# Performance work log

Hardware: AMD Instinct MI355X
Metric: run time of the kernel (lower is better)

The kernel has to match this reference:

```python
import jax, jax.numpy as jnp
import numpy as np

N, M, D, K = 8192, 16384, 512, 512
RESULT_BLUR = 0.01  # self.result_blur in the original module


def setup_inputs() -> dict:
    key = jax.random.key(0)
    k1, k2, k3, k4 = jax.random.split(key, 4)
    x = jax.random.normal(k1, (N, D), jnp.float32)          # current embeddings (feature_rows)
    cache_emb = jax.random.normal(k2, (M, D), jnp.float32)  # stacked prev_params embeddings
    cache_out = jax.random.normal(k3, (M, K), jnp.float32)  # feature_encoder.out_ts cached results
    W = jax.random.normal(k4, (D, K), jnp.float32) / np.sqrt(D)  # fallback equation weights
    b = jnp.zeros((K,), jnp.float32)
    return {"x": x, "cache_emb": cache_emb, "cache_out": cache_out, "W": W, "b": b}


def reference(x, cache_emb, cache_out, W, b):
    # --- fill_blur_vals (vmapped over query rows): L2 cdist + argmin retrieval ---
    x2 = jnp.sum(x * x, axis=1, keepdims=True)               # [N, 1]
    c2 = jnp.sum(cache_emb * cache_emb, axis=1)              # [M]
    d2 = x2 + c2[None, :] - 2.0 * (x @ cache_emb.T)          # [N, M]
    dists = jnp.sqrt(jnp.maximum(d2, 0.0))                   # jnp.linalg.norm(emb - cur, axis=1)
    idx = jnp.argmin(dists, axis=1)                          # [N]
    min_loss = jnp.take_along_axis(dists, idx[:, None], axis=1)[:, 0]
    use_cache = min_loss <= RESULT_BLUR                      # [N] bool
    # --- process_equation: cached result if blur hit, else run the equation ---
    run_out = x @ W + b                                      # [N, K] computed fallback
    cached = cache_out[idx]                                  # [N, K] gathered cached results
    return jnp.where(use_cache[:, None], cached, run_out)
```

## Files before the change

### kernel.cpp

```cpp
#include <hip/hip_runtime.h>
#include <hip/hip_bf16.h>
#include <hip/hip_fp8.h>
#include <cstdint>
#include <cstddef>


#define NQ 8192
#define MC 16384
#define DD 512
#define KK 512

typedef float f32x4 __attribute__((ext_vector_type(4)));
typedef __bf16 bf16x8 __attribute__((ext_vector_type(8)));
typedef short short8 __attribute__((ext_vector_type(8)));

#define MIN_OFF 0u
#define X2_OFF 65536u
#define C2_OFF 98304u
#define XB_OFF 163840u
#define XQ_OFF (XB_OFF + 8388608u)
#define CQ_OFF (XQ_OFF + 4194304u)
#define WT_OFF (CQ_OFF + 8388608u)
#define PART_OFF (WT_OFF + 524288u)

__device__ __forceinline__ short f2bf(float f) {
  unsigned int u = __float_as_uint(f);
  u += 0x7FFFu + ((u >> 16) & 1u);
  return (short)(u >> 16);
}

__device__ __forceinline__ void gload_lds16(const void* g, void* l) {
  __builtin_amdgcn_global_load_lds(
      (__attribute__((address_space(1))) void*)(g),
      (__attribute__((address_space(3))) void*)(l), 16, 0, 0);
}

__device__ __forceinline__ unsigned long long u64min(unsigned long long a,
                                                     unsigned long long b) {
  return a < b ? a : b;
}

template <int WRITE_BF16>
__global__ __launch_bounds__(256) void prep_rows(const float* __restrict__ src,
                                                 short* __restrict__ dstb,
                                                 unsigned char* __restrict__ dstq,
                                                 float* __restrict__ dst2) {
  const int lane = threadIdx.x & 63;
  const size_t row = (size_t)blockIdx.x * 4 + (threadIdx.x >> 6);
  const float4* p = (const float4*)(src + row * DD + lane * 8);
  float4 v0 = p[0], v1 = p[1];
  float v[8] = {v0.x, v0.y, v0.z, v0.w, v1.x, v1.y, v1.z, v1.w};
  unsigned long long pk = 0;
  float s = 0.f;
#pragma unroll
  for (int j = 0; j < 8; ++j) {
    __hip_fp8_e4m3 q(v[j]);
    float qf = (float)q;
    s += qf * qf;
    pk |= (unsigned long long)q.__x << (8 * j);
  }
  const int g = (lane & ~15) | ((lane & 15) ^ ((int)row & 15));
  *(unsigned long long*)(dstq + row * DD + g * 8) = pk;
  if (WRITE_BF16) {
    short8 o;
#pragma unroll
    for (int j = 0; j < 8; ++j) o[j] = f2bf(v[j]);
    *(short8*)(dstb + row * DD + lane * 8) = o;
  }
#pragma unroll
  for (int m = 32; m >= 1; m >>= 1) s += __shfl_xor(s, m, 64);
  if (lane == 0) dst2[row] = s;
}

__global__ __launch_bounds__(256) void prep_w(const float* __restrict__ W,
                                              short* __restrict__ wt) {
  __shared__ float t[64][65];
  const int bx = blockIdx.x, by = blockIdx.y;
#pragma unroll
  for (int i = 0; i < 16; ++i) {
    int idx = i * 256 + threadIdx.x;
    int r = idx >> 6, c = idx & 63;
    t[r][c] = W[(size_t)(by * 64 + r) * KK + bx * 64 + c];
  }
  __syncthreads();
#pragma unroll
  for (int i = 0; i < 16; ++i) {
    int idx = i * 256 + threadIdx.x;
    int r = idx >> 6, c = idx & 63;
    wt[(size_t)(bx * 64 + r) * DD + by * 64 + c] = f2bf(t[c][r]);
  }
}

__global__ __launch_bounds__(256, 4) void gemm_min(
    const unsigned char* __restrict__ xq, const unsigned char* __restrict__ cq,
    const float* __restrict__ x2, const float* __restrict__ c2,
    unsigned long long* __restrict__ part) {
  __shared__ unsigned char lA[128 * 128];
  __shared__ unsigned char lB[128 * 128];
  const int tid = threadIdx.x;
  const int lane = tid & 63;
  const int wid = tid >> 6;
  const int wr = wid >> 1, wc = wid & 1;
  const int cl = lane & 15, cr = lane >> 4;

  const int bid = blockIdx.x;
  const int xcd = bid & 7;
  const int k = bid >> 3;
  const int by = xcd * 8 + ((k >> 4) & 7);
  const int bx = ((k >> 7) << 4) | (k & 15);
  const size_t row0 = (size_t)by * 128;
  const size_t col0 = (size_t)bx * 128;

  unsigned goA[4], goB[4];
#pragma unroll
  for (int j = 0; j < 4; ++j) {
    const int ch = wid * 256 + j * 64 + lane;
    const int r = ch >> 3, c = ch & 7;
    goA[j] = (unsigned)((row0 + r) * DD + c * 16);
    goB[j] = (unsigned)((col0 + r) * DD + c * 16);
  }

  f32x4 acc[4][4];
#pragma unroll
  for (int m = 0; m < 4; ++m)
#pragma unroll
    for (int n = 0; n < 4; ++n) acc[m][n] = (f32x4)0.0f;

  const unsigned char* lAr = lA + (wr * 64 + cl) * 128;
  const unsigned char* lBr = lB + (wc * 64 + cl) * 128;
  int sl[4];
#pragma unroll
  for (int ks = 0; ks < 4; ++ks) sl[ks] = (((ks * 4 + cr) ^ cl) << 3);

  for (int kt = 0; kt < DD / 128; ++kt) {
    const unsigned kb = (unsigned)kt * 128;
#pragma unroll
    for (int j = 0; j < 4; ++j) {
      gload_lds16(xq + goA[j] + kb, lA + (wid * 256 + j * 64) * 16);
      gload_lds16(cq + goB[j] + kb, lB + (wid * 256 + j * 64) * 16);
    }
    __syncthreads();
#pragma unroll
    for (int ks = 0; ks < 4; ++ks) {
      long a[4], b[4];
#pragma unroll
      for (int m = 0; m < 4; ++m)
        a[m] = *(const long*)(lAr + m * 2048 + sl[ks]);
#pragma unroll
      for (int n = 0; n < 4; ++n)
        b[n] = *(const long*)(lBr + n * 2048 + sl[ks]);
#pragma unroll
      for (int m = 0; m < 4; ++m)
#pragma unroll
        for (int n = 0; n < 4; ++n)
          acc[m][n] = __builtin_amdgcn_mfma_f32_16x16x32_fp8_fp8(
              a[m], b[n], acc[m][n], 0, 0, 0);
    }
    __syncthreads();
  }

  unsigned long long* ls = (unsigned long long*)lA;
  float c2v[4];
#pragma unroll
  for (int n = 0; n < 4; ++n) c2v[n] = c2[col0 + wc * 64 + n * 16 + cl];
#pragma unroll
  for (int m = 0; m < 4; ++m) {
#pragma unroll
    for (int r = 0; r < 4; ++r) {
      const int row_local = wr * 64 + m * 16 + cr * 4 + r;
      const float xv = x2[row0 + row_local];
      unsigned long long best = ~0ull;
#pragma unroll
      for (int n = 0; n < 4; ++n) {
        float d2 = fmaxf(xv + c2v[n] - 2.0f * acc[m][n][r], 0.0f);
        unsigned int col = (unsigned int)(col0 + wc * 64 + n * 16 + cl);
        unsigned long long key =
            ((unsigned long long)__float_as_uint(d2) << 32) | col;
        best = u64min(best, key);
      }
#pragma unroll
      for (int msk = 8; msk >= 1; msk >>= 1) {
        unsigned long long o = __shfl_xor(best, msk, 64);
        best = u64min(best, o);
      }
      if (cl == 0) ls[row_local * 2 + wc] = best;
    }
  }
  __syncthreads();
  if (tid < 128) {
    unsigned long long b = u64min(ls[tid * 2 + 0], ls[tid * 2 + 1]);
    atomicMin(&part[(size_t)(row0 + tid) * 64 + (bx >> 1)], b);
  }
}

__global__ __launch_bounds__(256) void reduce_mink(
    const unsigned long long* __restrict__ part,
    unsigned long long* __restrict__ mink) {
  const int row = blockIdx.x * 256 + threadIdx.x;
  const unsigned long long* p = part + (size_t)row * 64;
  unsigned long long best = ~0ull;
#pragma unroll
  for (int j = 0; j < 64; ++j) best = best < p[j] ? best : p[j];
  mink[row] = best;
}

__device__ __forceinline__ void stage_offs(unsigned go[4], size_t grow0,
                                           int wid, int lane) {
#pragma unroll
  for (int j = 0; j < 4; ++j) {
    const int ch = wid * 256 + j * 64 + lane;
    const int r = ch >> 3;
    const int c = (ch & 7) ^ (r & 7);
    go[j] = (unsigned)((grow0 + (size_t)r) * (DD * 2) + c * 16);
  }
}

__device__ __forceinline__ void stage_tile(const char* base,
                                           const unsigned go[4], unsigned kb,
                                           char* lds, int wid) {
#pragma unroll
  for (int j = 0; j < 4; ++j)
    gload_lds16(base + go[j] + kb, lds + (wid * 256 + j * 64) * 16);
}

__device__ __forceinline__ bf16x8 ld_frag(const short* lrow0, int m, int ks,
                                          int cr, int cl) {
  const int slot = (ks * 4 + cr) ^ (cl & 7);
  return *(const bf16x8*)(lrow0 + m * 16 * 64 + slot * 8);
}

__global__ __launch_bounds__(256, 3) void gemm_out(
    const short* __restrict__ xb, const short* __restrict__ wt,
    const float* __restrict__ bias, const float* __restrict__ cache_out,
    const unsigned long long* __restrict__ mink, float* __restrict__ out) {
  __shared__ short lA[128 * 64];
  __shared__ short lB[128 * 64];
  const int tid = threadIdx.x;
  const int lane = tid & 63;
  const int wid = tid >> 6;
  const int wr = wid >> 1, wc = wid & 1;
  const int cl = lane & 15, cr = lane >> 4;
  const size_t row0 = (size_t)blockIdx.y * 128;
  const size_t col0 = (size_t)blockIdx.x * 128;

  unsigned goA[4], goB[4];
  stage_offs(goA, row0, wid, lane);
  stage_offs(goB, col0, wid, lane);
  const char* xbp = (const char*)xb;
  const char* wtp = (const char*)wt;

  f32x4 acc[4][4];
#pragma unroll
  for (int m = 0; m < 4; ++m)
#pragma unroll
    for (int n = 0; n < 4; ++n) acc[m][n] = (f32x4)0.0f;

  const short* lArow = lA + (wr * 64 + cl) * 64;
  const short* lBrow = lB + (wc * 64 + cl) * 64;

  for (int kt = 0; kt < DD / 64; ++kt) {
    stage_tile(xbp, goA, (unsigned)kt * 128, (char*)lA, wid);
    stage_tile(wtp, goB, (unsigned)kt * 128, (char*)lB, wid);
    __syncthreads();
#pragma unroll
    for (int ks = 0; ks < 2; ++ks) {
      bf16x8 a[4], b[4];
#pragma unroll
      for (int m = 0; m < 4; ++m) a[m] = ld_frag(lArow, m, ks, cr, cl);
#pragma unroll
      for (int n = 0; n < 4; ++n) b[n] = ld_frag(lBrow, n, ks, cr, cl);
#pragma unroll
      for (int m = 0; m < 4; ++m)
#pragma unroll
        for (int n = 0; n < 4; ++n)
          acc[m][n] = __builtin_amdgcn_mfma_f32_16x16x32_bf16(a[m], b[n],
                                                              acc[m][n], 0, 0, 0);
    }
    __syncthreads();
  }

#pragma unroll
  for (int m = 0; m < 4; ++m) {
#pragma unroll
    for (int r = 0; r < 4; ++r) {
      const size_t row = row0 + wr * 64 + m * 16 + cr * 4 + r;
      const unsigned long long key = mink[row];
      const float d2 = __uint_as_float((unsigned int)(key >> 32));
      const bool usec = (d2 <= 1e-4f);
      const unsigned int idx = (unsigned int)(key & 0xFFFFFFFFu);
#pragma unroll
      for (int n = 0; n < 4; ++n) {
        const size_t col = col0 + wc * 64 + n * 16 + cl;
        float v = acc[m][n][r] + bias[col];
        if (usec) v = cache_out[(size_t)idx * KK + col];
        out[row * KK + col] = v;
      }
    }
  }
}

extern "C" void kernel_launch(void* const* d_in, const int* in_sizes, int n_in,
                              void* d_out, int out_size, void* d_ws,
                              size_t ws_size, hipStream_t stream) {
  const float* x = (const float*)d_in[0];
  const float* cache_emb = (const float*)d_in[1];
  const float* cache_out = (const float*)d_in[2];
  const float* W = (const float*)d_in[3];
  const float* bias = (const float*)d_in[4];
  float* out = (float*)d_out;
  char* ws = (char*)d_ws;

  unsigned long long* mink = (unsigned long long*)(ws + MIN_OFF);
  float* x2 = (float*)(ws + X2_OFF);
  float* c2 = (float*)(ws + C2_OFF);
  short* xb = (short*)(ws + XB_OFF);
  unsigned char* xq = (unsigned char*)(ws + XQ_OFF);
  unsigned char* cq = (unsigned char*)(ws + CQ_OFF);
  short* wt = (short*)(ws + WT_OFF);
  unsigned long long* part = (unsigned long long*)(ws + PART_OFF);

  hipMemsetAsync(part, 0xFF, (size_t)NQ * 64 * 8, stream);
  prep_rows<1><<<NQ / 4, 256, 0, stream>>>(x, xb, xq, x2);
  prep_rows<0><<<MC / 4, 256, 0, stream>>>(cache_emb, nullptr, cq, c2);
  prep_w<<<dim3(KK / 64, DD / 64), 256, 0, stream>>>(W, wt);
  gemm_min<<<(NQ / 128) * (MC / 128), 256, 0, stream>>>(xq, cq, x2, c2, part);
  reduce_mink<<<NQ / 256, 256, 0, stream>>>(part, mink);
  gemm_out<<<dim3(KK / 128, NQ / 128), 256, 0, stream>>>(xb, wt, bias,
                                                         cache_out, mink, out);
}
```

Measured before the change: 176.8 us.

## Store fp8 operands in K-tiled panel layout and double-buffer LDS loads

The prep kernel now writes the fp8 quantized rows as contiguous 128-row by 64-byte K-panels with an XOR swizzle, so each stage of the distance GEMM loads fully contiguous 8KB chunks. The GEMM switches from a single 128-wide K tile with two syncthreads per step to eight 64-wide K steps with double-buffered LDS. The next stage is issued before waiting on the current one using explicit vmcnt waits. This aims to overlap global-to-LDS transfers with MFMA work and simplify address generation, at the cost of more barriers and tighter reliance on manual waitcnt correctness.

```diff
diff --git a/kernel.cpp b/kernel.cpp
--- a/kernel.cpp
+++ b/kernel.cpp
@@ -59,8 +59,11 @@
     s += qf * qf;
     pk |= (unsigned long long)q.__x << (8 * j);
   }
-  const int g = (lane & ~15) | ((lane & 15) ^ ((int)row & 15));
-  *(unsigned long long*)(dstq + row * DD + g * 8) = pk;
+  const int kt = lane >> 3, gl = lane & 7;
+  const int rl = (int)row & 127;
+  const size_t panel = row >> 7;
+  *(unsigned long long*)(dstq + (panel * 8 + kt) * 8192 + rl * 64 +
+                         ((gl ^ (rl & 7)) << 3)) = pk;
   if (WRITE_BF16) {
     short8 o;
 #pragma unroll
@@ -95,8 +98,7 @@
     const unsigned char* __restrict__ xq, const unsigned char* __restrict__ cq,
     const float* __restrict__ x2, const float* __restrict__ c2,
     unsigned long long* __restrict__ part) {
-  __shared__ unsigned char lA[128 * 128];
-  __shared__ unsigned char lB[128 * 128];
+  __shared__ unsigned char L[2][2][8192];
   const int tid = threadIdx.x;
   const int lane = tid & 63;
   const int wid = tid >> 6;
@@ -111,14 +113,8 @@
   const size_t row0 = (size_t)by * 128;
   const size_t col0 = (size_t)bx * 128;
 
-  unsigned goA[4], goB[4];
-#pragma unroll
-  for (int j = 0; j < 4; ++j) {
-    const int ch = wid * 256 + j * 64 + lane;
-    const int r = ch >> 3, c = ch & 7;
-    goA[j] = (unsigned)((row0 + r) * DD + c * 16);
-    goB[j] = (unsigned)((col0 + r) * DD + c * 16);
-  }
+  const unsigned char* tA = xq + (size_t)by * 65536;
+  const unsigned char* tB = cq + (size_t)bx * 65536;
 
   f32x4 acc[4][4];
 #pragma unroll
@@ -126,29 +122,37 @@
 #pragma unroll
     for (int n = 0; n < 4; ++n) acc[m][n] = (f32x4)0.0f;
 
-  const unsigned char* lAr = lA + (wr * 64 + cl) * 128;
-  const unsigned char* lBr = lB + (wc * 64 + cl) * 128;
-  int sl[4];
-#pragma unroll
-  for (int ks = 0; ks < 4; ++ks) sl[ks] = (((ks * 4 + cr) ^ cl) << 3);
-
-  for (int kt = 0; kt < DD / 128; ++kt) {
-    const unsigned kb = (unsigned)kt * 128;
-#pragma unroll
-    for (int j = 0; j < 4; ++j) {
-      gload_lds16(xq + goA[j] + kb, lA + (wid * 256 + j * 64) * 16);
-      gload_lds16(cq + goB[j] + kb, lB + (wid * 256 + j * 64) * 16);
-    }
-    __syncthreads();
-#pragma unroll
-    for (int ks = 0; ks < 4; ++ks) {
+#define STAGE(buf, kt)                                                     \
+  do {                                                                     \
+    gload_lds16(tA + (kt) * 8192 + tid * 16, &L[buf][0][tid * 16]);        \
+    gload_lds16(tA + (kt) * 8192 + 4096 + tid * 16,                        \
+                &L[buf][0][4096 + tid * 16]);                              \
+    gload_lds16(tB + (kt) * 8192 + tid * 16, &L[buf][1][tid * 16]);        \
+    gload_lds16(tB + (kt) * 8192 + 4096 + tid * 16,                        \
+                &L[buf][1][4096 + tid * 16]);                              \
+  } while (0)
+
+  int cur = 0;
+  STAGE(0, 0);
+  for (int kt = 0; kt < 8; ++kt) {
+    if (kt < 7) {
+      STAGE(cur ^ 1, kt + 1);
+      asm volatile("s_waitcnt vmcnt(4)" ::: "memory");
+    } else {
+      asm volatile("s_waitcnt vmcnt(0)" ::: "memory");
+    }
+    __builtin_amdgcn_s_barrier();
+    __builtin_amdgcn_sched_barrier(0);
+    const unsigned char* lAr = &L[cur][0][(wr * 64 + cl) * 64];
+    const unsigned char* lBr = &L[cur][1][(wc * 64 + cl) * 64];
+#pragma unroll
+    for (int ks = 0; ks < 2; ++ks) {
+      const int sl = ((ks * 4 + cr) ^ (cl & 7)) << 3;
       long a[4], b[4];
 #pragma unroll
-      for (int m = 0; m < 4; ++m)
-        a[m] = *(const long*)(lAr + m * 2048 + sl[ks]);
-#pragma unroll
-      for (int n = 0; n < 4; ++n)
-        b[n] = *(const long*)(lBr + n * 2048 + sl[ks]);
+      for (int m = 0; m < 4; ++m) a[m] = *(const long*)(lAr + m * 1024 + sl);
+#pragma unroll
+      for (int n = 0; n < 4; ++n) b[n] = *(const long*)(lBr + n * 1024 + sl);
 #pragma unroll
       for (int m = 0; m < 4; ++m)
 #pragma unroll
@@ -156,10 +160,12 @@
           acc[m][n] = __builtin_amdgcn_mfma_f32_16x16x32_fp8_fp8(
               a[m], b[n], acc[m][n], 0, 0, 0);
     }
-    __syncthreads();
-  }
-
-  unsigned long long* ls = (unsigned long long*)lA;
+    __builtin_amdgcn_s_barrier();
+    cur ^= 1;
+  }
+#undef STAGE
+
+  unsigned long long* ls = (unsigned long long*)&L[0][0][0];
   float c2v[4];
 #pragma unroll
   for (int n = 0; n < 4; ++n) c2v[n] = c2[col0 + wc * 64 + n * 16 + cl];
```

Measured after the change: 186.2 us. 1.05x slower.
